# Kernel tuning notes

Hardware: AMD Instinct MI355X
Metric: run time of the kernel (lower is better)

The kernel has to match this reference:

```python
import jax, jax.numpy as jnp
import numpy as np

N = 50000
E = 800000
G = 64  # number of graphs in each batch
IN_DIM = 128
HID = 64
NEG_SLOPE = 0.2


def _glorot(key, shape):
    fan = shape[0] + shape[-1] if len(shape) == 2 else int(np.prod(shape[1:])) + shape[-1]
    lim = float(np.sqrt(6.0 / fan))
    return jax.random.uniform(key, shape, jnp.float32, -lim, lim)


def setup_inputs() -> dict:
    key = jax.random.key(0)
    ks = jax.random.split(key, 16)
    x1 = jax.random.normal(ks[0], (N, IN_DIM), jnp.float32)
    x2 = jax.random.normal(ks[1], (N, IN_DIM), jnp.float32)
    edge_index1 = jax.random.randint(ks[2], (2, E), 0, N, jnp.int64)
    edge_index2 = jax.random.randint(ks[3], (2, E), 0, N, jnp.int64)
    batch1 = jnp.sort(jax.random.randint(ks[4], (N,), 0, G, jnp.int64))
    batch2 = jnp.sort(jax.random.randint(ks[5], (N,), 0, G, jnp.int64))
    # conv1: GATConv(IN_DIM, HID, heads=4)
    W1 = _glorot(ks[6], (IN_DIM, 4 * HID))
    a_src1 = _glorot(ks[7], (1, 4, HID))
    a_dst1 = _glorot(ks[8], (1, 4, HID))
    b1 = jnp.zeros((4 * HID,), jnp.float32)
    # conv2: GATConv(4*HID, HID, heads=1)
    W2 = _glorot(ks[9], (4 * HID, HID))
    a_src2 = _glorot(ks[10], (1, 1, HID))
    a_dst2 = _glorot(ks[11], (1, 1, HID))
    b2 = jnp.zeros((HID,), jnp.float32)
    return {"x1": x1, "edge_index1": edge_index1, "batch1": batch1,
            "x2": x2, "edge_index2": edge_index2, "batch2": batch2,
            "W1": W1, "a_src1": a_src1, "a_dst1": a_dst1, "b1": b1,
            "W2": W2, "a_src2": a_src2, "a_dst2": a_dst2, "b2": b2}


def gat_conv(x, src, dst, W, a_src, a_dst, b, n_nodes, heads, out_dim):
    """PyG GATConv with add_self_loops=True, negative_slope=0.2, concat=True."""
    h = (x @ W).reshape(n_nodes, heads, out_dim)            # [N,H,D]
    alpha_s = jnp.sum(h * a_src, axis=-1)                   # [N,H]
    alpha_d = jnp.sum(h * a_dst, axis=-1)                   # [N,H]
    e = alpha_s[src] + alpha_d[dst]                         # [E',H]
    e = jax.nn.leaky_relu(e, NEG_SLOPE)
    # segment softmax over incoming edges of each destination node
    e_max = jax.ops.segment_max(e, dst, num_segments=n_nodes)
    ex = jnp.exp(e - e_max[dst])
    denom = jax.ops.segment_sum(ex, dst, num_segments=n_nodes)
    alpha = ex / (denom[dst] + 1e-16)                       # [E',H]
    msg = h[src] * alpha[:, :, None]                        # [E',H,D]
    out = jax.ops.segment_sum(msg, dst, num_segments=n_nodes)
    return out.reshape(n_nodes, heads * out_dim) + b


def embed(x, edge_index, batch, W1, a_src1, a_dst1, b1, W2, a_src2, a_dst2, b2):
    loops = jnp.arange(N, dtype=edge_index.dtype)
    src = jnp.concatenate([edge_index[0], loops])
    dst = jnp.concatenate([edge_index[1], loops])
    h = jax.nn.elu(gat_conv(x, src, dst, W1, a_src1, a_dst1, b1, N, 4, HID))
    h = jax.nn.elu(gat_conv(h, src, dst, W2, a_src2, a_dst2, b2, N, 1, HID))
    # global_mean_pool over graph ids
    sums = jax.ops.segment_sum(h, batch, num_segments=G)
    cnt = jax.ops.segment_sum(jnp.ones((N,), h.dtype), batch, num_segments=G)
    return sums / jnp.maximum(cnt, 1.0)[:, None]


def reference(x1, edge_index1, batch1, x2, edge_index2, batch2,
              W1, a_src1, a_dst1, b1, W2, a_src2, a_dst2, b2):
    emb1 = embed(x1, edge_index1, batch1, W1, a_src1, a_dst1, b1, W2, a_src2, a_dst2, b2)
    emb2 = embed(x2, edge_index2, batch2, W1, a_src1, a_dst1, b1, W2, a_src2, a_dst2, b2)
    return (emb1, emb2)
```

## Files before the change

kernel.cpp:

```cpp
#include <hip/hip_runtime.h>
#include <cstdint>
#include <cstddef>

#define NNODES 50000
#define NEDGES 800000
#define NGR    64
#define INDIM  128
#define HIDD   64

typedef __attribute__((ext_vector_type(8))) short bf16x8;
typedef __attribute__((ext_vector_type(4))) float f32x4;

__device__ __forceinline__ float lrelu(float x) { return x > 0.f ? x : 0.2f * x; }
__device__ __forceinline__ float eluf(float x)  { return x > 0.f ? x : expm1f(x); }
__device__ __forceinline__ float bf2f(unsigned short u) {
    return __uint_as_float((unsigned int)u << 16);
}
__device__ __forceinline__ unsigned short f2bf(float x) {
    unsigned int u = __float_as_uint(x);
    return (unsigned short)((u + 0x7fffu + ((u >> 16) & 1u)) >> 16);
}
__device__ __forceinline__ float lo16(unsigned int u) { return __uint_as_float(u << 16); }
__device__ __forceinline__ float hi16(unsigned int u) { return __uint_as_float(u & 0xffff0000u); }

__global__ void cvt_f2b(const float* __restrict__ in, unsigned short* __restrict__ out, int n4) {
    int i = blockIdx.x * 256 + threadIdx.x;
    if (i < n4) {
        float4 v = ((const float4*)in)[i];
        ushort4 o;
        o.x = f2bf(v.x); o.y = f2bf(v.y); o.z = f2bf(v.z); o.w = f2bf(v.w);
        ((ushort4*)out)[i] = o;
    }
}

__global__ void count_dst(const int* __restrict__ ei0, const int* __restrict__ ei1,
                          int* __restrict__ cnt, int E, int N) {
    const int* ei = blockIdx.y ? ei1 : ei0;
    int* c = cnt + blockIdx.y * N;
    int e = blockIdx.x * 256 + threadIdx.x;
    if (e < E) atomicAdd(&c[ei[E + e]], 1);
}

__global__ __launch_bounds__(256) void scan_part(const int* __restrict__ cnt,
                                                 int* __restrict__ psum, int n) {
    __shared__ int ws[4];
    const int* c = cnt + blockIdx.y * n;
    int* p = psum + blockIdx.y * 256;
    int lane = threadIdx.x & 63, w = threadIdx.x >> 6;
    int i = blockIdx.x * 256 + threadIdx.x;
    int v = (i < n) ? c[i] : 0;
    #pragma unroll
    for (int off = 32; off >= 1; off >>= 1) v += __shfl_xor(v, off, 64);
    if (lane == 0) ws[w] = v;
    __syncthreads();
    if (threadIdx.x == 0) p[blockIdx.x] = ws[0] + ws[1] + ws[2] + ws[3];
}

__global__ __launch_bounds__(256) void scan_tops(int* __restrict__ psum,
                                                 int* __restrict__ rp, int nb, int n) {
    __shared__ int wsum[4];
    int* p = psum + blockIdx.x * 256;
    int* r = rp + blockIdx.x * (n + 1);
    int tid = threadIdx.x, lane = tid & 63, w = tid >> 6;
    int v = (tid < nb) ? p[tid] : 0;
    int x = v;
    #pragma unroll
    for (int off = 1; off < 64; off <<= 1) {
        int t = __shfl_up(x, off, 64);
        if (lane >= off) x += t;
    }
    if (lane == 63) wsum[w] = x;
    __syncthreads();
    int add = 0;
    for (int k = 0; k < w; k++) add += wsum[k];
    int incl = x + add;
    if (tid < nb) p[tid] = incl - v;
    if (tid == nb - 1) r[n] = incl;
}

__global__ __launch_bounds__(256) void scan_fin(const int* __restrict__ cnt,
                                                const int* __restrict__ psum,
                                                int* __restrict__ rp, int n) {
    __shared__ int wsum[4];
    const int* c = cnt + blockIdx.y * n;
    const int* p = psum + blockIdx.y * 256;
    int* r = rp + blockIdx.y * (n + 1);
    int tid = threadIdx.x, lane = tid & 63, w = tid >> 6;
    int i = blockIdx.x * 256 + tid;
    int v = (i < n) ? c[i] : 0;
    int x = v;
    #pragma unroll
    for (int off = 1; off < 64; off <<= 1) {
        int t = __shfl_up(x, off, 64);
        if (lane >= off) x += t;
    }
    if (lane == 63) wsum[w] = x;
    __syncthreads();
    int add = p[blockIdx.x];
    for (int k = 0; k < w; k++) add += wsum[k];
    if (i < n) r[i] = x + add - v;
}

__global__ void fill_csr(const int* __restrict__ ei0, const int* __restrict__ ei1,
                         const int* __restrict__ rp, int* __restrict__ fc,
                         int* __restrict__ col, int E, int N) {
    int g = blockIdx.y;
    const int* ei = g ? ei1 : ei0;
    const int* r = rp + g * (N + 1);
    int* f = fc + g * N;
    int* cl = col + (size_t)g * E;
    int e = blockIdx.x * 256 + threadIdx.x;
    if (e < E) {
        int s = ei[e];
        int d = ei[E + e];
        int pos = atomicAdd(&f[d], 1);
        cl[r[d] + pos] = s;
    }
}

template<int BN, int WM, int WN, bool AF32>
__global__ __launch_bounds__(256) void gemm_mfma(const void* __restrict__ A0,
                                                 const void* __restrict__ A1,
                                                 size_t Ags,
                                                 const unsigned short* __restrict__ Bw,
                                                 unsigned short* __restrict__ C,
                                                 size_t Cgs,
                                                 int M, int K, int N,
                                                 const float* __restrict__ a_src,
                                                 const float* __restrict__ a_dst,
                                                 float* __restrict__ as_o,
                                                 float* __restrict__ ad_o,
                                                 int hstride, int ags) {
    constexpr int BM = 128, BK = 64;
    constexpr int MI = WM / 16, NI = WN / 16;
    constexpr int LDA = BK + 8;
    __shared__ unsigned short Asm[BM * LDA];
    __shared__ unsigned short Bsm[BN * LDA];
    int gph = blockIdx.z;
    const float* Af = (const float*)(gph ? A1 : A0);
    const unsigned short* Ab = (const unsigned short*)A0 + (size_t)gph * Ags;
    unsigned short* Cg = C + (size_t)gph * Cgs;
    float* aso = as_o + (size_t)gph * ags;
    float* ado = ad_o + (size_t)gph * ags;
    int tid = threadIdx.x;
    int lane = tid & 63, wave = tid >> 6;
    int l15 = lane & 15, quad = lane >> 4;
    int wm0, wn0;
    if (BN == 128) { wm0 = (wave >> 1) * 64; wn0 = (wave & 1) * 64; }
    else           { wm0 = wave * 32;        wn0 = 0; }
    int row0 = blockIdx.x * BM;
    int c0 = blockIdx.y * BN;

    f32x4 acc[MI][NI];
    #pragma unroll
    for (int mi = 0; mi < MI; mi++)
        #pragma unroll
        for (int ni = 0; ni < NI; ni++)
            acc[mi][ni] = (f32x4){0.f, 0.f, 0.f, 0.f};

    for (int k0 = 0; k0 < K; k0 += BK) {
        #pragma unroll
        for (int q = 0; q < BM / 32; q++) {
            int idx = q * 256 + tid;
            int r = idx >> 3, kc = idx & 7;
            int row = row0 + r;
            if (AF32) {
                float4 v0 = make_float4(0.f, 0.f, 0.f, 0.f), v1 = v0;
                if (row < M) {
                    v0 = *(const float4*)(Af + (size_t)row * K + k0 + kc * 8);
                    v1 = *(const float4*)(Af + (size_t)row * K + k0 + kc * 8 + 4);
                }
                unsigned short t[8] = {f2bf(v0.x), f2bf(v0.y), f2bf(v0.z), f2bf(v0.w),
                                       f2bf(v1.x), f2bf(v1.y), f2bf(v1.z), f2bf(v1.w)};
                *(uint4*)&Asm[r * LDA + kc * 8] = *(uint4*)t;
            } else {
                uint4 v = make_uint4(0u, 0u, 0u, 0u);
                if (row < M) v = *(const uint4*)(Ab + (size_t)row * K + k0 + kc * 8);
                *(uint4*)&Asm[r * LDA + kc * 8] = v;
            }
        }
        #pragma unroll
        for (int q = 0; q < BN / 32; q++) {
            int idx = q * 256 + tid;
            int n  = idx & (BN - 1);
            int kc = idx / BN;
            unsigned short tmp[8];
            #pragma unroll
            for (int j = 0; j < 8; j++)
                tmp[j] = Bw[(size_t)(k0 + kc * 8 + j) * N + c0 + n];
            *(uint4*)&Bsm[n * LDA + kc * 8] = *(uint4*)tmp;
        }
        __syncthreads();
        #pragma unroll
        for (int kb = 0; kb < 2; kb++) {
            bf16x8 af[MI], bfr[NI];
            #pragma unroll
            for (int mi = 0; mi < MI; mi++)
                af[mi] = *(bf16x8*)&Asm[(wm0 + mi * 16 + l15) * LDA + kb * 32 + quad * 8];
            #pragma unroll
            for (int ni = 0; ni < NI; ni++)
                bfr[ni] = *(bf16x8*)&Bsm[(wn0 + ni * 16 + l15) * LDA + kb * 32 + quad * 8];
            #pragma unroll
            for (int mi = 0; mi < MI; mi++)
                #pragma unroll
                for (int ni = 0; ni < NI; ni++)
                    acc[mi][ni] = __builtin_amdgcn_mfma_f32_16x16x32_bf16(
                        af[mi], bfr[ni], acc[mi][ni], 0, 0, 0);
        }
        __syncthreads();
    }
    #pragma unroll
    for (int mi = 0; mi < MI; mi++) {
        #pragma unroll
        for (int r = 0; r < 4; r++) {
            int row = row0 + wm0 + mi * 16 + quad * 4 + r;
            if (row < M) {
                #pragma unroll
                for (int ni = 0; ni < NI; ni++) {
                    int colg = c0 + wn0 + ni * 16 + l15;
                    Cg[(size_t)row * N + colg] = f2bf(acc[mi][ni][r]);
                }
            }
        }
    }
    int headc = (c0 + wn0) >> 6;
    float a_s[NI], a_d[NI];
    #pragma unroll
    for (int ni = 0; ni < NI; ni++) {
        a_s[ni] = a_src[headc * 64 + ni * 16 + l15];
        a_d[ni] = a_dst[headc * 64 + ni * 16 + l15];
    }
    #pragma unroll
    for (int mi = 0; mi < MI; mi++) {
        #pragma unroll
        for (int r = 0; r < 4; r++) {
            float ps = 0.f, pd = 0.f;
            #pragma unroll
            for (int ni = 0; ni < NI; ni++) {
                ps += acc[mi][ni][r] * a_s[ni];
                pd += acc[mi][ni][r] * a_d[ni];
            }
            #pragma unroll
            for (int off = 1; off < 16; off <<= 1) {
                ps += __shfl_xor(ps, off, 64);
                pd += __shfl_xor(pd, off, 64);
            }
            int row = row0 + wm0 + mi * 16 + quad * 4 + r;
            if (l15 == 0 && row < M) {
                aso[row * hstride + headc] = ps;
                ado[row * hstride + headc] = pd;
            }
        }
    }
}

__global__ __launch_bounds__(256) void agg_h4(const unsigned short* __restrict__ h,
                                              size_t hgs,
                                              const float* __restrict__ as_,
                                              const float* __restrict__ ad_, int ags,
                                              const int* __restrict__ rp,
                                              const int* __restrict__ col,
                                              const float* __restrict__ bias,
                                              unsigned short* __restrict__ out,
                                              size_t ogs, int n, int E) {
    int gph = blockIdx.y;
    const uint4* h4 = (const uint4*)(h + (size_t)gph * hgs);
    const float* as = as_ + (size_t)gph * ags;
    const float* adp = ad_ + (size_t)gph * ags;
    const int* r = rp + gph * (n + 1);
    const int* cl = col + (size_t)gph * E;
    unsigned short* og = out + (size_t)gph * ogs;

    int wave = threadIdx.x >> 6, lane = threadIdx.x & 63;
    int node = blockIdx.x * 4 + wave;
    if (node >= n) return;
    int p = lane >> 5;
    int c = lane & 31;
    int headc = c >> 3;
    int l15 = lane & 15, quad = lane >> 4;
    float adv_q = adp[node * 4 + quad];
    float w0 = __expf(lrelu(as[node * 4 + headc] + adp[node * 4 + headc]));
    float m0 = (p == 0) ? w0 : 0.f;
    uint4 hu = h4[(size_t)node * 32 + c];
    float den = m0;
    float a0 = lo16(hu.x) * m0, a1 = hi16(hu.x) * m0;
    float a2 = lo16(hu.y) * m0, a3 = hi16(hu.y) * m0;
    float a4 = lo16(hu.z) * m0, a5 = hi16(hu.z) * m0;
    float a6 = lo16(hu.w) * m0, a7 = hi16(hu.w) * m0;
    int beg = __builtin_amdgcn_readfirstlane(r[node]);
    int end = __builtin_amdgcn_readfirstlane(r[node + 1]);
    int hbase = headc << 4;
    for (int j = beg; j < end; j += 16) {
        int m = end - j; if (m > 16) m = 16;
        int colv = cl[j + (l15 < m ? l15 : m - 1)];
        float wl = __expf(lrelu(as[colv * 4 + quad] + adv_q));
        for (int base = 0; base < m; base += 2) {
            int e = base + p;
            int ec = e < m ? e : m - 1;
            float we = __shfl(wl, hbase | ec);
            if (e >= m) we = 0.f;
            int s = __shfl(colv, ec);
            uint4 u = h4[(size_t)s * 32 + c];
            den += we;
            a0 += lo16(u.x) * we; a1 += hi16(u.x) * we;
            a2 += lo16(u.y) * we; a3 += hi16(u.y) * we;
            a4 += lo16(u.z) * we; a5 += hi16(u.z) * we;
            a6 += lo16(u.w) * we; a7 += hi16(u.w) * we;
        }
    }
    den += __shfl_xor(den, 32);
    a0 += __shfl_xor(a0, 32); a1 += __shfl_xor(a1, 32);
    a2 += __shfl_xor(a2, 32); a3 += __shfl_xor(a3, 32);
    a4 += __shfl_xor(a4, 32); a5 += __shfl_xor(a5, 32);
    a6 += __shfl_xor(a6, 32); a7 += __shfl_xor(a7, 32);
    if (p == 0) {
        float rden = 1.f / (den + 1e-16f);
        float4 b0 = ((const float4*)bias)[c * 2];
        float4 b1 = ((const float4*)bias)[c * 2 + 1];
        unsigned short t[8];
        t[0] = f2bf(eluf(a0 * rden + b0.x)); t[1] = f2bf(eluf(a1 * rden + b0.y));
        t[2] = f2bf(eluf(a2 * rden + b0.z)); t[3] = f2bf(eluf(a3 * rden + b0.w));
        t[4] = f2bf(eluf(a4 * rden + b1.x)); t[5] = f2bf(eluf(a5 * rden + b1.y));
        t[6] = f2bf(eluf(a6 * rden + b1.z)); t[7] = f2bf(eluf(a7 * rden + b1.w));
        ((uint4*)(og + (size_t)node * 256))[c] = *(uint4*)t;
    }
}

__global__ __launch_bounds__(256) void agg_h1(const unsigned short* __restrict__ h,
                                              size_t hgs,
                                              const float* __restrict__ as_,
                                              const float* __restrict__ ad_,
                                              const int* __restrict__ rp,
                                              const int* __restrict__ col,
                                              const float* __restrict__ bias,
                                              float* __restrict__ out,
                                              size_t ogs, int n, int E) {
    int gph = blockIdx.y;
    const uint4* h4 = (const uint4*)(h + (size_t)gph * hgs);
    const float* as = as_ + (size_t)gph * n;
    const float* adp = ad_ + (size_t)gph * n;
    const int* r = rp + gph * (n + 1);
    const int* cl = col + (size_t)gph * E;
    float* og = out + (size_t)gph * ogs;

    int wave = threadIdx.x >> 6, lane = threadIdx.x & 63;
    int node = blockIdx.x * 4 + wave;
    if (node >= n) return;
    int p = lane >> 3;
    int c = lane & 7;
    float adv = adp[node];
    float w0 = __expf(lrelu(as[node] + adv));
    float m0 = (p == 0) ? w0 : 0.f;
    uint4 hu = h4[(size_t)node * 8 + c];
    float den = m0;
    float a0 = lo16(hu.x) * m0, a1 = hi16(hu.x) * m0;
    float a2 = lo16(hu.y) * m0, a3 = hi16(hu.y) * m0;
    float a4 = lo16(hu.z) * m0, a5 = hi16(hu.z) * m0;
    float a6 = lo16(hu.w) * m0, a7 = hi16(hu.w) * m0;
    int beg = __builtin_amdgcn_readfirstlane(r[node]);
    int end = __builtin_amdgcn_readfirstlane(r[node + 1]);
    for (int j = beg; j < end; j += 64) {
        int m = end - j; if (m > 64) m = 64;
        int colv = cl[j + (lane < m ? lane : m - 1)];
        float wl = __expf(lrelu(as[colv] + adv));
        for (int base = 0; base < m; base += 8) {
            int e = base + p;
            int ec = e < m ? e : m - 1;
            float we = __shfl(wl, ec);
            if (e >= m) we = 0.f;
            int s = __shfl(colv, ec);
            uint4 u = h4[(size_t)s * 8 + c];
            den += we;
            a0 += lo16(u.x) * we; a1 += hi16(u.x) * we;
            a2 += lo16(u.y) * we; a3 += hi16(u.y) * we;
            a4 += lo16(u.z) * we; a5 += hi16(u.z) * we;
            a6 += lo16(u.w) * we; a7 += hi16(u.w) * we;
        }
    }
    #pragma unroll
    for (int off = 8; off < 64; off <<= 1) {
        den += __shfl_xor(den, off);
        a0 += __shfl_xor(a0, off); a1 += __shfl_xor(a1, off);
        a2 += __shfl_xor(a2, off); a3 += __shfl_xor(a3, off);
        a4 += __shfl_xor(a4, off); a5 += __shfl_xor(a5, off);
        a6 += __shfl_xor(a6, off); a7 += __shfl_xor(a7, off);
    }
    if (p == 0) {
        float rden = 1.f / (den + 1e-16f);
        float4 b0 = ((const float4*)bias)[c * 2];
        float4 b1 = ((const float4*)bias)[c * 2 + 1];
        float4 o0, o1;
        o0.x = eluf(a0 * rden + b0.x); o0.y = eluf(a1 * rden + b0.y);
        o0.z = eluf(a2 * rden + b0.z); o0.w = eluf(a3 * rden + b0.w);
        o1.x = eluf(a4 * rden + b1.x); o1.y = eluf(a5 * rden + b1.y);
        o1.z = eluf(a6 * rden + b1.z); o1.w = eluf(a7 * rden + b1.w);
        float* orow = og + (size_t)node * 64 + c * 8;
        *(float4*)orow = o0;
        *(float4*)(orow + 4) = o1;
    }
}

__device__ __forceinline__ int lbound(const int* __restrict__ a, int n, int key) {
    int lo = 0, hi = n;
    while (lo < hi) {
        int mid = (lo + hi) >> 1;
        if (a[mid] < key) lo = mid + 1; else hi = mid;
    }
    return lo;
}

__global__ __launch_bounds__(256) void pool_mean(const float* __restrict__ g2,
                                                 size_t ggs,
                                                 const int* __restrict__ b0,
                                                 const int* __restrict__ b1,
                                                 float* __restrict__ out, int n) {
    __shared__ float red[4][64];
    __shared__ int bnds[2];
    int gph = blockIdx.y;
    const int* batch = gph ? b1 : b0;
    const float* gg = g2 + (size_t)gph * ggs;
    float* og = out + (size_t)gph * NGR * HIDD;
    int g = blockIdx.x;
    if (threadIdx.x < 2) bnds[threadIdx.x] = lbound(batch, n, g + (int)threadIdx.x);
    __syncthreads();
    int s = bnds[0], e = bnds[1];
    int lane = threadIdx.x & 63, wave = threadIdx.x >> 6;
    float acc = 0.f;
    for (int i = s + wave; i < e; i += 4)
        acc += gg[(size_t)i * 64 + lane];
    red[wave][lane] = acc;
    __syncthreads();
    if (wave == 0) {
        float sum = red[0][lane] + red[1][lane] + red[2][lane] + red[3][lane];
        og[g * 64 + lane] = sum / fmaxf((float)(e - s), 1.0f);
    }
}

extern "C" void kernel_launch(void* const* d_in, const int* in_sizes, int n_in,
                              void* d_out, int out_size, void* d_ws, size_t ws_size,
                              hipStream_t stream) {
    const int N = NNODES, E = NEDGES;

    const float* x1 = (const float*)d_in[0];
    const float* x2 = (const float*)d_in[3];
    const int* ei1v = (const int*)d_in[1];
    const int* ei2v = (const int*)d_in[4];
    const int* ba1  = (const int*)d_in[2];
    const int* ba2  = (const int*)d_in[5];
    const float* W1     = (const float*)d_in[6];
    const float* a_src1 = (const float*)d_in[7];
    const float* a_dst1 = (const float*)d_in[8];
    const float* b1     = (const float*)d_in[9];
    const float* W2     = (const float*)d_in[10];
    const float* a_src2 = (const float*)d_in[11];
    const float* a_dst2 = (const float*)d_in[12];
    const float* b2     = (const float*)d_in[13];

    char* ws = (char*)d_ws;
    size_t off = 0;
    auto carve = [&](size_t bytes) -> char* {
        char* p = ws + off;
        off = (off + bytes + 255) & ~(size_t)255;
        return p;
    };
    char* R1 = carve((size_t)2 * N * 256 * 2);
    char* R2 = carve((size_t)2 * N * 256 * 2);
    char* R3 = carve((size_t)2 * N * 64 * 2);
    int*   col  = (int*)carve((size_t)2 * E * 4);
    int*   rp   = (int*)carve((size_t)2 * (N + 1) * 4);
    int*   cntN = (int*)carve((size_t)2 * N * 4);
    int*   psum = (int*)carve(2 * 256 * 4);
    float* as1  = (float*)carve((size_t)2 * N * 4 * 4);
    float* ad1  = (float*)carve((size_t)2 * N * 4 * 4);
    float* as2  = (float*)carve((size_t)2 * N * 4);
    float* ad2  = (float*)carve((size_t)2 * N * 4);
    unsigned short* W1b = (unsigned short*)carve(INDIM * 256 * 2);
    unsigned short* W2b = (unsigned short*)carve(256 * HIDD * 2);

    unsigned short* h1 = (unsigned short*)R1;
    unsigned short* g1 = (unsigned short*)R2;
    unsigned short* h2 = (unsigned short*)R3;
    float* g2 = (float*)R1;

    float* outF = (float*)d_out;

    const int nodeBlocks = (N + 3) / 4;
    const int nb = (N + 255) / 256;
    const int eb = (E + 255) / 256;

    cvt_f2b<<<(INDIM * 256 / 4 + 255) / 256, 256, 0, stream>>>(W1, W1b, INDIM * 256 / 4);
    cvt_f2b<<<(256 * HIDD / 4 + 255) / 256, 256, 0, stream>>>(W2, W2b, 256 * HIDD / 4);

    hipMemsetAsync(cntN, 0, (size_t)2 * N * 4, stream);
    count_dst<<<dim3(eb, 2), 256, 0, stream>>>(ei1v, ei2v, cntN, E, N);
    scan_part<<<dim3(nb, 2), 256, 0, stream>>>(cntN, psum, N);
    scan_tops<<<2, 256, 0, stream>>>(psum, rp, nb, N);
    scan_fin<<<dim3(nb, 2), 256, 0, stream>>>(cntN, psum, rp, N);
    hipMemsetAsync(cntN, 0, (size_t)2 * N * 4, stream);
    fill_csr<<<dim3(eb, 2), 256, 0, stream>>>(ei1v, ei2v, rp, cntN, col, E, N);

    gemm_mfma<128, 64, 64, true><<<dim3(391, 2, 2), 256, 0, stream>>>(
        x1, x2, 0, W1b, h1, (size_t)N * 256, N, INDIM, 256,
        a_src1, a_dst1, as1, ad1, 4, N * 4);
    agg_h4<<<dim3(nodeBlocks, 2), 256, 0, stream>>>(h1, (size_t)N * 256, as1, ad1, N * 4,
                                                    rp, col, b1, g1, (size_t)N * 256, N, E);

    gemm_mfma<64, 32, 64, false><<<dim3(391, 1, 2), 256, 0, stream>>>(
        g1, nullptr, (size_t)N * 256, W2b, h2, (size_t)N * 64, N, 256, HIDD,
        a_src2, a_dst2, as2, ad2, 1, N);
    agg_h1<<<dim3(nodeBlocks, 2), 256, 0, stream>>>(h2, (size_t)N * 64, as2, ad2,
                                                    rp, col, b2, g2, (size_t)N * 64, N, E);

    pool_mean<<<dim3(NGR, 2), 256, 0, stream>>>(g2, (size_t)N * 64, ba1, ba2, outF, N);
}
```

Baseline: 575.3 us.

## Software-pipeline GAT aggregation gathers and widen per-lane feature slices in layer 0

In the layer-0 aggregation kernel, each lane now handles 16 features (two uint4 loads) and the wave processes four edges at a time instead of two. In both aggregation kernels the next edge's feature row and the next chunk's column indices and source attention scores are prefetched before the current ones are accumulated. The aim is to hide gather latency and issue more memory requests in flight. The cost is more live registers (16 accumulators plus the prefetched vectors), which can lower occupancy.

```diff
diff --git a/kernel.cpp b/kernel.cpp
--- a/kernel.cpp
+++ b/kernel.cpp
@@ -274,55 +274,108 @@
     int wave = threadIdx.x >> 6, lane = threadIdx.x & 63;
     int node = blockIdx.x * 4 + wave;
     if (node >= n) return;
-    int p = lane >> 5;
-    int c = lane & 31;
-    int headc = c >> 3;
-    int l15 = lane & 15, quad = lane >> 4;
-    float adv_q = adp[node * 4 + quad];
+    int p = lane >> 4;
+    int c = lane & 15;
+    int headc = c >> 2;
+    float adv_q = adp[node * 4 + p];
     float w0 = __expf(lrelu(as[node * 4 + headc] + adp[node * 4 + headc]));
     float m0 = (p == 0) ? w0 : 0.f;
-    uint4 hu = h4[(size_t)node * 32 + c];
+    uint4 hu0 = h4[(size_t)node * 32 + 2 * c];
+    uint4 hu1 = h4[(size_t)node * 32 + 2 * c + 1];
     float den = m0;
-    float a0 = lo16(hu.x) * m0, a1 = hi16(hu.x) * m0;
-    float a2 = lo16(hu.y) * m0, a3 = hi16(hu.y) * m0;
-    float a4 = lo16(hu.z) * m0, a5 = hi16(hu.z) * m0;
-    float a6 = lo16(hu.w) * m0, a7 = hi16(hu.w) * m0;
+    float a0  = lo16(hu0.x) * m0, a1  = hi16(hu0.x) * m0;
+    float a2  = lo16(hu0.y) * m0, a3  = hi16(hu0.y) * m0;
+    float a4  = lo16(hu0.z) * m0, a5  = hi16(hu0.z) * m0;
+    float a6  = lo16(hu0.w) * m0, a7  = hi16(hu0.w) * m0;
+    float a8  = lo16(hu1.x) * m0, a9  = hi16(hu1.x) * m0;
+    float a10 = lo16(hu1.y) * m0, a11 = hi16(hu1.y) * m0;
+    float a12 = lo16(hu1.z) * m0, a13 = hi16(hu1.z) * m0;
+    float a14 = lo16(hu1.w) * m0, a15 = hi16(hu1.w) * m0;
     int beg = __builtin_amdgcn_readfirstlane(r[node]);
     int end = __builtin_amdgcn_readfirstlane(r[node + 1]);
     int hbase = headc << 4;
-    for (int j = beg; j < end; j += 16) {
-        int m = end - j; if (m > 16) m = 16;
-        int colv = cl[j + (l15 < m ? l15 : m - 1)];
-        float wl = __expf(lrelu(as[colv * 4 + quad] + adv_q));
-        for (int base = 0; base < m; base += 2) {
-            int e = base + p;
-            int ec = e < m ? e : m - 1;
-            float we = __shfl(wl, hbase | ec);
-            if (e >= m) we = 0.f;
-            int s = __shfl(colv, ec);
-            uint4 u = h4[(size_t)s * 32 + c];
+    int j = beg;
+    int m = end - j; if (m > 16) m = 16;
+    int colv = 0; float asv = 0.f;
+    if (j < end) {
+        colv = cl[j + (c < m ? c : m - 1)];
+        asv = as[colv * 4 + p];
+    }
+    while (j < end) {
+        int jn = j + 16;
+        int mn = end - jn; if (mn > 16) mn = 16;
+        int colv_n = 0; float asv_n = 0.f;
+        if (mn > 0) {
+            colv_n = cl[jn + (c < mn ? c : mn - 1)];
+            asv_n = as[colv_n * 4 + p];
+        }
+        float wl = __expf(lrelu(asv + adv_q));
+        int e0 = p;
+        int ec = e0 < m ? e0 : m - 1;
+        float we = __shfl(wl, hbase | ec);
+        if (e0 >= m) we = 0.f;
+        int s = __shfl(colv, ec);
+        uint4 u0 = h4[(size_t)s * 32 + 2 * c];
+        uint4 u1 = h4[(size_t)s * 32 + 2 * c + 1];
+        for (int base = 4; base < m; base += 4) {
+            int e2 = base + p;
+            int ec2 = e2 < m ? e2 : m - 1;
+            float we2 = __shfl(wl, hbase | ec2);
+            if (e2 >= m) we2 = 0.f;
+            int s2 = __shfl(colv, ec2);
+            uint4 v0 = h4[(size_t)s2 * 32 + 2 * c];
+            uint4 v1 = h4[(size_t)s2 * 32 + 2 * c + 1];
             den += we;
-            a0 += lo16(u.x) * we; a1 += hi16(u.x) * we;
-            a2 += lo16(u.y) * we; a3 += hi16(u.y) * we;
-            a4 += lo16(u.z) * we; a5 += hi16(u.z) * we;
-            a6 += lo16(u.w) * we; a7 += hi16(u.w) * we;
-        }
-    }
-    den += __shfl_xor(den, 32);
-    a0 += __shfl_xor(a0, 32); a1 += __shfl_xor(a1, 32);
-    a2 += __shfl_xor(a2, 32); a3 += __shfl_xor(a3, 32);
-    a4 += __shfl_xor(a4, 32); a5 += __shfl_xor(a5, 32);
-    a6 += __shfl_xor(a6, 32); a7 += __shfl_xor(a7, 32);
+            a0  += lo16(u0.x) * we; a1  += hi16(u0.x) * we;
+            a2  += lo16(u0.y) * we; a3  += hi16(u0.y) * we;
+            a4  += lo16(u0.z) * we; a5  += hi16(u0.z) * we;
+            a6  += lo16(u0.w) * we; a7  += hi16(u0.w) * we;
+            a8  += lo16(u1.x) * we; a9  += hi16(u1.x) * we;
+            a10 += lo16(u1.y) * we; a11 += hi16(u1.y) * we;
+            a12 += lo16(u1.z) * we; a13 += hi16(u1.z) * we;
+            a14 += lo16(u1.w) * we; a15 += hi16(u1.w) * we;
+            we = we2; u0 = v0; u1 = v1;
+        }
+        den += we;
+        a0  += lo16(u0.x) * we; a1  += hi16(u0.x) * we;
+        a2  += lo16(u0.y) * we; a3  += hi16(u0.y) * we;
+        a4  += lo16(u0.z) * we; a5  += hi16(u0.z) * we;
+        a6  += lo16(u0.w) * we; a7  += hi16(u0.w) * we;
+        a8  += lo16(u1.x) * we; a9  += hi16(u1.x) * we;
+        a10 += lo16(u1.y) * we; a11 += hi16(u1.y) * we;
+        a12 += lo16(u1.z) * we; a13 += hi16(u1.z) * we;
+        a14 += lo16(u1.w) * we; a15 += hi16(u1.w) * we;
+        j = jn; m = mn; colv = colv_n; asv = asv_n;
+    }
+    #pragma unroll
+    for (int off = 16; off < 64; off <<= 1) {
+        den += __shfl_xor(den, off);
+        a0  += __shfl_xor(a0,  off); a1  += __shfl_xor(a1,  off);
+        a2  += __shfl_xor(a2,  off); a3  += __shfl_xor(a3,  off);
+        a4  += __shfl_xor(a4,  off); a5  += __shfl_xor(a5,  off);
+        a6  += __shfl_xor(a6,  off); a7  += __shfl_xor(a7,  off);
+        a8  += __shfl_xor(a8,  off); a9  += __shfl_xor(a9,  off);
+        a10 += __shfl_xor(a10, off); a11 += __shfl_xor(a11, off);
+        a12 += __shfl_xor(a12, off); a13 += __shfl_xor(a13, off);
+        a14 += __shfl_xor(a14, off); a15 += __shfl_xor(a15, off);
+    }
     if (p == 0) {
         float rden = 1.f / (den + 1e-16f);
-        float4 b0 = ((const float4*)bias)[c * 2];
-        float4 b1 = ((const float4*)bias)[c * 2 + 1];
-        unsigned short t[8];
-        t[0] = f2bf(eluf(a0 * rden + b0.x)); t[1] = f2bf(eluf(a1 * rden + b0.y));
-        t[2] = f2bf(eluf(a2 * rden + b0.z)); t[3] = f2bf(eluf(a3 * rden + b0.w));
-        t[4] = f2bf(eluf(a4 * rden + b1.x)); t[5] = f2bf(eluf(a5 * rden + b1.y));
-        t[6] = f2bf(eluf(a6 * rden + b1.z)); t[7] = f2bf(eluf(a7 * rden + b1.w));
-        ((uint4*)(og + (size_t)node * 256))[c] = *(uint4*)t;
+        const float4* b4 = (const float4*)bias;
+        float4 b0 = b4[c * 4], b1 = b4[c * 4 + 1];
+        float4 b2 = b4[c * 4 + 2], b3 = b4[c * 4 + 3];
+        unsigned short t[16];
+        t[0]  = f2bf(eluf(a0  * rden + b0.x)); t[1]  = f2bf(eluf(a1  * rden + b0.y));
+        t[2]  = f2bf(eluf(a2  * rden + b0.z)); t[3]  = f2bf(eluf(a3  * rden + b0.w));
+        t[4]  = f2bf(eluf(a4  * rden + b1.x)); t[5]  = f2bf(eluf(a5  * rden + b1.y));
+        t[6]  = f2bf(eluf(a6  * rden + b1.z)); t[7]  = f2bf(eluf(a7  * rden + b1.w));
+        t[8]  = f2bf(eluf(a8  * rden + b2.x)); t[9]  = f2bf(eluf(a9  * rden + b2.y));
+        t[10] = f2bf(eluf(a10 * rden + b2.z)); t[11] = f2bf(eluf(a11 * rden + b2.w));
+        t[12] = f2bf(eluf(a12 * rden + b3.x)); t[13] = f2bf(eluf(a13 * rden + b3.y));
+        t[14] = f2bf(eluf(a14 * rden + b3.z)); t[15] = f2bf(eluf(a15 * rden + b3.w));
+        uint4* orow = (uint4*)(og + (size_t)node * 256);
+        orow[2 * c]     = *(uint4*)&t[0];
+        orow[2 * c + 1] = *(uint4*)&t[8];
     }
 }
 
@@ -359,23 +412,48 @@
     float a6 = lo16(hu.w) * m0, a7 = hi16(hu.w) * m0;
     int beg = __builtin_amdgcn_readfirstlane(r[node]);
     int end = __builtin_amdgcn_readfirstlane(r[node + 1]);
-    for (int j = beg; j < end; j += 64) {
-        int m = end - j; if (m > 64) m = 64;
-        int colv = cl[j + (lane < m ? lane : m - 1)];
-        float wl = __expf(lrelu(as[colv] + adv));
-        for (int base = 0; base < m; base += 8) {
-            int e = base + p;
-            int ec = e < m ? e : m - 1;
-            float we = __shfl(wl, ec);
-            if (e >= m) we = 0.f;
-            int s = __shfl(colv, ec);
-            uint4 u = h4[(size_t)s * 8 + c];
+    int j = beg;
+    int m = end - j; if (m > 64) m = 64;
+    int colv = 0; float asv = 0.f;
+    if (j < end) {
+        colv = cl[j + (lane < m ? lane : m - 1)];
+        asv = as[colv];
+    }
+    while (j < end) {
+        int jn = j + 64;
+        int mn = end - jn; if (mn > 64) mn = 64;
+        int colv_n = 0; float asv_n = 0.f;
+        if (mn > 0) {
+            colv_n = cl[jn + (lane < mn ? lane : mn - 1)];
+            asv_n = as[colv_n];
+        }
+        float wl = __expf(lrelu(asv + adv));
+        int e0 = p;
+        int ec = e0 < m ? e0 : m - 1;
+        float we = __shfl(wl, ec);
+        if (e0 >= m) we = 0.f;
+        int s = __shfl(colv, ec);
+        uint4 u = h4[(size_t)s * 8 + c];
+        for (int base = 8; base < m; base += 8) {
+            int e2 = base + p;
+            int ec2 = e2 < m ? e2 : m - 1;
+            float we2 = __shfl(wl, ec2);
+            if (e2 >= m) we2 = 0.f;
+            int s2 = __shfl(colv, ec2);
+            uint4 u2 = h4[(size_t)s2 * 8 + c];
             den += we;
             a0 += lo16(u.x) * we; a1 += hi16(u.x) * we;
             a2 += lo16(u.y) * we; a3 += hi16(u.y) * we;
             a4 += lo16(u.z) * we; a5 += hi16(u.z) * we;
             a6 += lo16(u.w) * we; a7 += hi16(u.w) * we;
-        }
+            we = we2; u = u2;
+        }
+        den += we;
+        a0 += lo16(u.x) * we; a1 += hi16(u.x) * we;
+        a2 += lo16(u.y) * we; a3 += hi16(u.y) * we;
+        a4 += lo16(u.z) * we; a5 += hi16(u.z) * we;
+        a6 += lo16(u.w) * we; a7 += hi16(u.w) * we;
+        j = jn; m = mn; colv = colv_n; asv = asv_n;
     }
     #pragma unroll
     for (int off = 8; off < 64; off <<= 1) {
```

New measurement: 571.7 us. No clear change (-0.6%).

## Aggregate raw inputs before projection in first GAT layer and switch to fp16

Applied to the files above, without the earlier changes.

Layer one is reordered so neighbor aggregation runs over the 128-wide fp16 input features instead of the 256-wide projected features. Per-head attention logits come from x times a precomputed W1·a vector, and the per-head aggregated inputs are then multiplied by W1 in a GEMM that also applies bias and ELU. This cuts the bytes gathered per edge in the largest gather, but it writes four per-head aggregated copies and adds extra kernels. The change also moves all 16-bit storage and MFMA from bf16 to fp16, which adds overflow and precision risk.

```diff
diff --git a/kernel.cpp b/kernel.cpp
--- a/kernel.cpp
+++ b/kernel.cpp
@@ -8,28 +8,90 @@
 #define INDIM  128
 #define HIDD   64
 
-typedef __attribute__((ext_vector_type(8))) short bf16x8;
+typedef __attribute__((ext_vector_type(8))) _Float16 f16x8;
+typedef __attribute__((ext_vector_type(2))) _Float16 half2v;
 typedef __attribute__((ext_vector_type(4))) float f32x4;
 
 __device__ __forceinline__ float lrelu(float x) { return x > 0.f ? x : 0.2f * x; }
 __device__ __forceinline__ float eluf(float x)  { return x > 0.f ? x : expm1f(x); }
-__device__ __forceinline__ float bf2f(unsigned short u) {
-    return __uint_as_float((unsigned int)u << 16);
-}
-__device__ __forceinline__ unsigned short f2bf(float x) {
-    unsigned int u = __float_as_uint(x);
-    return (unsigned short)((u + 0x7fffu + ((u >> 16) & 1u)) >> 16);
-}
-__device__ __forceinline__ float lo16(unsigned int u) { return __uint_as_float(u << 16); }
-__device__ __forceinline__ float hi16(unsigned int u) { return __uint_as_float(u & 0xffff0000u); }
-
-__global__ void cvt_f2b(const float* __restrict__ in, unsigned short* __restrict__ out, int n4) {
+__device__ __forceinline__ unsigned short f2h(float x) {
+    _Float16 h = (_Float16)x;
+    return __builtin_bit_cast(unsigned short, h);
+}
+__device__ __forceinline__ float h2f(unsigned short u) {
+    return (float)__builtin_bit_cast(_Float16, u);
+}
+__device__ __forceinline__ float h2lo(unsigned int u) {
+    half2v h = __builtin_bit_cast(half2v, u);
+    return (float)h.x;
+}
+__device__ __forceinline__ float h2hi(unsigned int u) {
+    half2v h = __builtin_bit_cast(half2v, u);
+    return (float)h.y;
+}
+
+__global__ void cvt_f2h(const float* __restrict__ in, unsigned short* __restrict__ out, int n4) {
     int i = blockIdx.x * 256 + threadIdx.x;
     if (i < n4) {
         float4 v = ((const float4*)in)[i];
         ushort4 o;
-        o.x = f2bf(v.x); o.y = f2bf(v.y); o.z = f2bf(v.z); o.w = f2bf(v.w);
+        o.x = f2h(v.x); o.y = f2h(v.y); o.z = f2h(v.z); o.w = f2h(v.w);
         ((ushort4*)out)[i] = o;
+    }
+}
+
+__global__ __launch_bounds__(256) void proj_ws(const float* __restrict__ W1f,
+                                               const float* __restrict__ a_src,
+                                               const float* __restrict__ a_dst,
+                                               float* __restrict__ proj) {
+    int o = blockIdx.x * 256 + threadIdx.x;
+    if (o >= 1024) return;
+    int sd = o >> 9, h = (o >> 7) & 3, k = o & 127;
+    const float* av = sd ? a_dst : a_src;
+    float s = 0.f;
+    #pragma unroll 8
+    for (int d = 0; d < 64; d++)
+        s += W1f[k * 256 + h * 64 + d] * av[h * 64 + d];
+    proj[o] = s;
+}
+
+__global__ __launch_bounds__(256) void cvt_xa(const float* __restrict__ x0,
+                                              const float* __restrict__ x1,
+                                              const float* __restrict__ proj,
+                                              unsigned short* __restrict__ x16,
+                                              float* __restrict__ as1,
+                                              float* __restrict__ ad1, int n) {
+    int gph = blockIdx.y;
+    const float* xf = (gph ? x1 : x0);
+    unsigned short* xo = x16 + (size_t)gph * n * 128;
+    float* aso = as1 + (size_t)gph * n * 4;
+    float* ado = ad1 + (size_t)gph * n * 4;
+    int wave = threadIdx.x >> 6, lane = threadIdx.x & 63;
+    int node = blockIdx.x * 4 + wave;
+    if (node >= n) return;
+    float2 v = *(const float2*)(xf + (size_t)node * 128 + lane * 2);
+    ushort2 t; t.x = f2h(v.x); t.y = f2h(v.y);
+    *(unsigned int*)(xo + (size_t)node * 128 + lane * 2) =
+        __builtin_bit_cast(unsigned int, t);
+    float ps[4], pd[4];
+    #pragma unroll
+    for (int h = 0; h < 4; h++) {
+        float2 ws = *(const float2*)(proj + h * 128 + lane * 2);
+        float2 wd = *(const float2*)(proj + 512 + h * 128 + lane * 2);
+        ps[h] = v.x * ws.x + v.y * ws.y;
+        pd[h] = v.x * wd.x + v.y * wd.y;
+    }
+    #pragma unroll
+    for (int off = 1; off < 64; off <<= 1) {
+        #pragma unroll
+        for (int h = 0; h < 4; h++) {
+            ps[h] += __shfl_xor(ps[h], off, 64);
+            pd[h] += __shfl_xor(pd[h], off, 64);
+        }
+    }
+    if (lane == 0) {
+        *(float4*)(aso + node * 4) = make_float4(ps[0], ps[1], ps[2], ps[3]);
+        *(float4*)(ado + node * 4) = make_float4(pd[0], pd[1], pd[2], pd[3]);
     }
 }
 
@@ -118,9 +180,165 @@
     }
 }
 
-template<int BN, int WM, int WN, bool AF32>
-__global__ __launch_bounds__(256) void gemm_mfma(const void* __restrict__ A0,
-                                                 const void* __restrict__ A1,
+__global__ __launch_bounds__(256) void agg_x4(const unsigned short* __restrict__ x16,
+                                              const float* __restrict__ as_,
+                                              const float* __restrict__ ad_,
+                                              const int* __restrict__ rp,
+                                              const int* __restrict__ col,
+                                              unsigned short* __restrict__ z,
+                                              int n, int E, int gph) {
+    const unsigned short* xg = x16 + (size_t)gph * n * 128;
+    const float* as = as_ + (size_t)gph * n * 4;
+    const float* adp = ad_ + (size_t)gph * n * 4;
+    const int* r = rp + gph * (n + 1);
+    const int* cl = col + (size_t)gph * E;
+
+    int wave = threadIdx.x >> 6, lane = threadIdx.x & 63;
+    int node = blockIdx.x * 4 + wave;
+    if (node >= n) return;
+    int p = lane >> 5;
+    int c = lane & 31;
+    int l15 = lane & 15, quad = lane >> 4;
+    float adv_q = adp[node * 4 + quad];
+
+    float w0[4];
+    #pragma unroll
+    for (int h = 0; h < 4; h++)
+        w0[h] = __expf(lrelu(as[node * 4 + h] + adp[node * 4 + h]));
+    uint2 hu = *(const uint2*)(xg + (size_t)node * 128 + c * 4);
+    float x0 = h2lo(hu.x), x1v = h2hi(hu.x), x2v = h2lo(hu.y), x3v = h2hi(hu.y);
+    float den[4], acc[4][4];
+    #pragma unroll
+    for (int h = 0; h < 4; h++) {
+        float m0 = (p == 0) ? w0[h] : 0.f;
+        den[h] = m0;
+        acc[h][0] = x0 * m0; acc[h][1] = x1v * m0;
+        acc[h][2] = x2v * m0; acc[h][3] = x3v * m0;
+    }
+    int beg = __builtin_amdgcn_readfirstlane(r[node]);
+    int end = __builtin_amdgcn_readfirstlane(r[node + 1]);
+    for (int j = beg; j < end; j += 16) {
+        int m = end - j; if (m > 16) m = 16;
+        int colv = cl[j + (l15 < m ? l15 : m - 1)];
+        float wl = __expf(lrelu(as[colv * 4 + quad] + adv_q));
+        for (int base = 0; base < m; base += 2) {
+            int e = base + p;
+            int ec = e < m ? e : m - 1;
+            int s = __shfl(colv, ec);
+            uint2 u = *(const uint2*)(xg + (size_t)s * 128 + c * 4);
+            float f0 = h2lo(u.x), f1 = h2hi(u.x), f2v = h2lo(u.y), f3 = h2hi(u.y);
+            #pragma unroll
+            for (int h = 0; h < 4; h++) {
+                float we = __shfl(wl, (h << 4) | ec);
+                if (e >= m) we = 0.f;
+                den[h] += we;
+                acc[h][0] = fmaf(f0, we, acc[h][0]);
+                acc[h][1] = fmaf(f1, we, acc[h][1]);
+                acc[h][2] = fmaf(f2v, we, acc[h][2]);
+                acc[h][3] = fmaf(f3, we, acc[h][3]);
+            }
+        }
+    }
+    #pragma unroll
+    for (int h = 0; h < 4; h++) {
+        den[h] += __shfl_xor(den[h], 32);
+        #pragma unroll
+        for (int k = 0; k < 4; k++) acc[h][k] += __shfl_xor(acc[h][k], 32);
+    }
+    if (p == 0) {
+        #pragma unroll
+        for (int h = 0; h < 4; h++) {
+            float rden = 1.f / (den[h] + 1e-16f);
+            ushort4 t;
+            t.x = f2h(acc[h][0] * rden); t.y = f2h(acc[h][1] * rden);
+            t.z = f2h(acc[h][2] * rden); t.w = f2h(acc[h][3] * rden);
+            *(uint2*)(z + ((size_t)h * n + node) * 128 + c * 4) = *(uint2*)&t;
+        }
+    }
+}
+
+__global__ __launch_bounds__(256) void gemm_z(const unsigned short* __restrict__ z,
+                                              const unsigned short* __restrict__ W1h,
+                                              const float* __restrict__ bias,
+                                              unsigned short* __restrict__ g1,
+                                              int M, int gph) {
+    constexpr int BM = 128, BK = 64, LDA = BK + 8;
+    __shared__ unsigned short Asm[BM * LDA];
+    __shared__ unsigned short Bsm[64 * LDA];
+    int h = blockIdx.z;
+    const unsigned short* Az = z + (size_t)h * M * 128;
+    unsigned short* Cg = g1 + (size_t)gph * M * 256;
+    int c0 = h * 64;
+    int tid = threadIdx.x, lane = tid & 63, wave = tid >> 6;
+    int l15 = lane & 15, quad = lane >> 4;
+    int wm0 = wave * 32;
+    int row0 = blockIdx.x * BM;
+
+    f32x4 acc[2][4];
+    #pragma unroll
+    for (int mi = 0; mi < 2; mi++)
+        #pragma unroll
+        for (int ni = 0; ni < 4; ni++)
+            acc[mi][ni] = (f32x4){0.f, 0.f, 0.f, 0.f};
+
+    for (int k0 = 0; k0 < 128; k0 += BK) {
+        #pragma unroll
+        for (int q = 0; q < 4; q++) {
+            int idx = q * 256 + tid;
+            int r = idx >> 3, kc = idx & 7;
+            int row = row0 + r;
+            uint4 v = make_uint4(0u, 0u, 0u, 0u);
+            if (row < M) v = *(const uint4*)(Az + (size_t)row * 128 + k0 + kc * 8);
+            *(uint4*)&Asm[r * LDA + kc * 8] = v;
+        }
+        #pragma unroll
+        for (int q = 0; q < 2; q++) {
+            int idx = q * 256 + tid;
+            int n = idx & 63;
+            int kc = idx >> 6;
+            unsigned short tmp[8];
+            #pragma unroll
+            for (int j = 0; j < 8; j++)
+                tmp[j] = W1h[(size_t)(k0 + kc * 8 + j) * 256 + c0 + n];
+            *(uint4*)&Bsm[n * LDA + kc * 8] = *(uint4*)tmp;
+        }
+        __syncthreads();
+        #pragma unroll
+        for (int kb = 0; kb < 2; kb++) {
+            f16x8 af[2], bfr[4];
+            #pragma unroll
+            for (int mi = 0; mi < 2; mi++)
+                af[mi] = *(f16x8*)&Asm[(wm0 + mi * 16 + l15) * LDA + kb * 32 + quad * 8];
+            #pragma unroll
+            for (int ni = 0; ni < 4; ni++)
+                bfr[ni] = *(f16x8*)&Bsm[(ni * 16 + l15) * LDA + kb * 32 + quad * 8];
+            #pragma unroll
+            for (int mi = 0; mi < 2; mi++)
+                #pragma unroll
+                for (int ni = 0; ni < 4; ni++)
+                    acc[mi][ni] = __builtin_amdgcn_mfma_f32_16x16x32_f16(
+                        af[mi], bfr[ni], acc[mi][ni], 0, 0, 0);
+        }
+        __syncthreads();
+    }
+    #pragma unroll
+    for (int mi = 0; mi < 2; mi++) {
+        #pragma unroll
+        for (int r = 0; r < 4; r++) {
+            int row = row0 + wm0 + mi * 16 + quad * 4 + r;
+            if (row < M) {
+                #pragma unroll
+                for (int ni = 0; ni < 4; ni++) {
+                    int colg = c0 + ni * 16 + l15;
+                    Cg[(size_t)row * 256 + colg] = f2h(eluf(acc[mi][ni][r] + bias[colg]));
+                }
+            }
+        }
+    }
+}
+
+template<int BN, int WM, int WN>
+__global__ __launch_bounds__(256) void gemm_mfma(const unsigned short* __restrict__ A0,
                                                  size_t Ags,
                                                  const unsigned short* __restrict__ Bw,
                                                  unsigned short* __restrict__ C,
@@ -137,17 +355,14 @@
     __shared__ unsigned short Asm[BM * LDA];
     __shared__ unsigned short Bsm[BN * LDA];
     int gph = blockIdx.z;
-    const float* Af = (const float*)(gph ? A1 : A0);
-    const unsigned short* Ab = (const unsigned short*)A0 + (size_t)gph * Ags;
+    const unsigned short* Ab = A0 + (size_t)gph * Ags;
     unsigned short* Cg = C + (size_t)gph * Cgs;
     float* aso = as_o + (size_t)gph * ags;
     float* ado = ad_o + (size_t)gph * ags;
     int tid = threadIdx.x;
     int lane = tid & 63, wave = tid >> 6;
     int l15 = lane & 15, quad = lane >> 4;
-    int wm0, wn0;
-    if (BN == 128) { wm0 = (wave >> 1) * 64; wn0 = (wave & 1) * 64; }
-    else           { wm0 = wave * 32;        wn0 = 0; }
+    int wm0 = wave * 32, wn0 = 0;
     int row0 = blockIdx.x * BM;
     int c0 = blockIdx.y * BN;
 
@@ -164,20 +379,9 @@
             int idx = q * 256 + tid;
             int r = idx >> 3, kc = idx & 7;
             int row = row0 + r;
-            if (AF32) {
-                float4 v0 = make_float4(0.f, 0.f, 0.f, 0.f), v1 = v0;
-                if (row < M) {
-                    v0 = *(const float4*)(Af + (size_t)row * K + k0 + kc * 8);
-                    v1 = *(const float4*)(Af + (size_t)row * K + k0 + kc * 8 + 4);
-                }
-                unsigned short t[8] = {f2bf(v0.x), f2bf(v0.y), f2bf(v0.z), f2bf(v0.w),
-                                       f2bf(v1.x), f2bf(v1.y), f2bf(v1.z), f2bf(v1.w)};
-                *(uint4*)&Asm[r * LDA + kc * 8] = *(uint4*)t;
-            } else {
-                uint4 v = make_uint4(0u, 0u, 0u, 0u);
-                if (row < M) v = *(const uint4*)(Ab + (size_t)row * K + k0 + kc * 8);
-                *(uint4*)&Asm[r * LDA + kc * 8] = v;
-            }
+            uint4 v = make_uint4(0u, 0u, 0u, 0u);
+            if (row < M) v = *(const uint4*)(Ab + (size_t)row * K + k0 + kc * 8);
+            *(uint4*)&Asm[r * LDA + kc * 8] = v;
         }
         #pragma unroll
         for (int q = 0; q < BN / 32; q++) {
@@ -193,18 +397,18 @@
         __syncthreads();
         #pragma unroll
         for (int kb = 0; kb < 2; kb++) {
-            bf16x8 af[MI], bfr[NI];
+            f16x8 af[MI], bfr[NI];
             #pragma unroll
             for (int mi = 0; mi < MI; mi++)
-                af[mi] = *(bf16x8*)&Asm[(wm0 + mi * 16 + l15) * LDA + kb * 32 + quad * 8];
+                af[mi] = *(f16x8*)&Asm[(wm0 + mi * 16 + l15) * LDA + kb * 32 + quad * 8];
             #pragma unroll
             for (int ni = 0; ni < NI; ni++)
-                bfr[ni] = *(bf16x8*)&Bsm[(wn0 + ni * 16 + l15) * LDA + kb * 32 + quad * 8];
+                bfr[ni] = *(f16x8*)&Bsm[(wn0 + ni * 16 + l15) * LDA + kb * 32 + quad * 8];
             #pragma unroll
             for (int mi = 0; mi < MI; mi++)
                 #pragma unroll
                 for (int ni = 0; ni < NI; ni++)
-                    acc[mi][ni] = __builtin_amdgcn_mfma_f32_16x16x32_bf16(
+                    acc[mi][ni] = __builtin_amdgcn_mfma_f32_16x16x32_f16(
                         af[mi], bfr[ni], acc[mi][ni], 0, 0, 0);
         }
         __syncthreads();
@@ -218,7 +422,7 @@
                 #pragma unroll
                 for (int ni = 0; ni < NI; ni++) {
                     int colg = c0 + wn0 + ni * 16 + l15;
-                    Cg[(size_t)row * N + colg] = f2bf(acc[mi][ni][r]);
+                    Cg[(size_t)row * N + colg] = f2h(acc[mi][ni][r]);
                 }
             }
         }
@@ -251,78 +455,6 @@
                 ado[row * hstride + headc] = pd;
             }
         }
-    }
-}
-
-__global__ __launch_bounds__(256) void agg_h4(const unsigned short* __restrict__ h,
-                                              size_t hgs,
-                                              const float* __restrict__ as_,
-                                              const float* __restrict__ ad_, int ags,
-                                              const int* __restrict__ rp,
-                                              const int* __restrict__ col,
-                                              const float* __restrict__ bias,
-                                              unsigned short* __restrict__ out,
-                                              size_t ogs, int n, int E) {
-    int gph = blockIdx.y;
-    const uint4* h4 = (const uint4*)(h + (size_t)gph * hgs);
-    const float* as = as_ + (size_t)gph * ags;
-    const float* adp = ad_ + (size_t)gph * ags;
-    const int* r = rp + gph * (n + 1);
-    const int* cl = col + (size_t)gph * E;
-    unsigned short* og = out + (size_t)gph * ogs;
-
-    int wave = threadIdx.x >> 6, lane = threadIdx.x & 63;
-    int node = blockIdx.x * 4 + wave;
-    if (node >= n) return;
-    int p = lane >> 5;
-    int c = lane & 31;
-    int headc = c >> 3;
-    int l15 = lane & 15, quad = lane >> 4;
-    float adv_q = adp[node * 4 + quad];
-    float w0 = __expf(lrelu(as[node * 4 + headc] + adp[node * 4 + headc]));
-    float m0 = (p == 0) ? w0 : 0.f;
-    uint4 hu = h4[(size_t)node * 32 + c];
-    float den = m0;
-    float a0 = lo16(hu.x) * m0, a1 = hi16(hu.x) * m0;
-    float a2 = lo16(hu.y) * m0, a3 = hi16(hu.y) * m0;
-    float a4 = lo16(hu.z) * m0, a5 = hi16(hu.z) * m0;
-    float a6 = lo16(hu.w) * m0, a7 = hi16(hu.w) * m0;
-    int beg = __builtin_amdgcn_readfirstlane(r[node]);
-    int end = __builtin_amdgcn_readfirstlane(r[node + 1]);
-    int hbase = headc << 4;
-    for (int j = beg; j < end; j += 16) {
-        int m = end - j; if (m > 16) m = 16;
-        int colv = cl[j + (l15 < m ? l15 : m - 1)];
-        float wl = __expf(lrelu(as[colv * 4 + quad] + adv_q));
-        for (int base = 0; base < m; base += 2) {
-            int e = base + p;
-            int ec = e < m ? e : m - 1;
-            float we = __shfl(wl, hbase | ec);
-            if (e >= m) we = 0.f;
-            int s = __shfl(colv, ec);
-            uint4 u = h4[(size_t)s * 32 + c];
-            den += we;
-            a0 += lo16(u.x) * we; a1 += hi16(u.x) * we;
-            a2 += lo16(u.y) * we; a3 += hi16(u.y) * we;
-            a4 += lo16(u.z) * we; a5 += hi16(u.z) * we;
-            a6 += lo16(u.w) * we; a7 += hi16(u.w) * we;
-        }
-    }
-    den += __shfl_xor(den, 32);
-    a0 += __shfl_xor(a0, 32); a1 += __shfl_xor(a1, 32);
-    a2 += __shfl_xor(a2, 32); a3 += __shfl_xor(a3, 32);
-    a4 += __shfl_xor(a4, 32); a5 += __shfl_xor(a5, 32);
-    a6 += __shfl_xor(a6, 32); a7 += __shfl_xor(a7, 32);
-    if (p == 0) {
-        float rden = 1.f / (den + 1e-16f);
-        float4 b0 = ((const float4*)bias)[c * 2];
-        float4 b1 = ((const float4*)bias)[c * 2 + 1];
-        unsigned short t[8];
-        t[0] = f2bf(eluf(a0 * rden + b0.x)); t[1] = f2bf(eluf(a1 * rden + b0.y));
-        t[2] = f2bf(eluf(a2 * rden + b0.z)); t[3] = f2bf(eluf(a3 * rden + b0.w));
-        t[4] = f2bf(eluf(a4 * rden + b1.x)); t[5] = f2bf(eluf(a5 * rden + b1.y));
-        t[6] = f2bf(eluf(a6 * rden + b1.z)); t[7] = f2bf(eluf(a7 * rden + b1.w));
-        ((uint4*)(og + (size_t)node * 256))[c] = *(uint4*)t;
     }
 }
 
@@ -353,10 +485,10 @@
     float m0 = (p == 0) ? w0 : 0.f;
     uint4 hu = h4[(size_t)node * 8 + c];
     float den = m0;
-    float a0 = lo16(hu.x) * m0, a1 = hi16(hu.x) * m0;
-    float a2 = lo16(hu.y) * m0, a3 = hi16(hu.y) * m0;
-    float a4 = lo16(hu.z) * m0, a5 = hi16(hu.z) * m0;
-    float a6 = lo16(hu.w) * m0, a7 = hi16(hu.w) * m0;
+    float a0 = h2lo(hu.x) * m0, a1 = h2hi(hu.x) * m0;
+    float a2 = h2lo(hu.y) * m0, a3 = h2hi(hu.y) * m0;
+    float a4 = h2lo(hu.z) * m0, a5 = h2hi(hu.z) * m0;
+    float a6 = h2lo(hu.w) * m0, a7 = h2hi(hu.w) * m0;
     int beg = __builtin_amdgcn_readfirstlane(r[node]);
     int end = __builtin_amdgcn_readfirstlane(r[node + 1]);
     for (int j = beg; j < end; j += 64) {
@@ -371,10 +503,10 @@
             int s = __shfl(colv, ec);
             uint4 u = h4[(size_t)s * 8 + c];
             den += we;
-            a0 += lo16(u.x) * we; a1 += hi16(u.x) * we;
-            a2 += lo16(u.y) * we; a3 += hi16(u.y) * we;
-            a4 += lo16(u.z) * we; a5 += hi16(u.z) * we;
-            a6 += lo16(u.w) * we; a7 += hi16(u.w) * we;
+            a0 = fmaf(h2lo(u.x), we, a0); a1 = fmaf(h2hi(u.x), we, a1);
+            a2 = fmaf(h2lo(u.y), we, a2); a3 = fmaf(h2hi(u.y), we, a3);
+            a4 = fmaf(h2lo(u.z), we, a4); a5 = fmaf(h2hi(u.z), we, a5);
+            a6 = fmaf(h2lo(u.w), we, a6); a7 = fmaf(h2hi(u.w), we, a7);
         }
     }
     #pragma unroll
@@ -463,9 +595,9 @@
         off = (off + bytes + 255) & ~(size_t)255;
         return p;
     };
-    char* R1 = carve((size_t)2 * N * 256 * 2);
-    char* R2 = carve((size_t)2 * N * 256 * 2);
-    char* R3 = carve((size_t)2 * N * 64 * 2);
+    unsigned short* x16 = (unsigned short*)carve((size_t)2 * N * 128 * 2);
+    char* Rz = carve((size_t)4 * N * 128 * 2);
+    unsigned short* g1 = (unsigned short*)carve((size_t)2 * N * 256 * 2);
     int*   col  = (int*)carve((size_t)2 * E * 4);
     int*   rp   = (int*)carve((size_t)2 * (N + 1) * 4);
     int*   cntN = (int*)carve((size_t)2 * N * 4);
@@ -474,13 +606,13 @@
     float* ad1  = (float*)carve((size_t)2 * N * 4 * 4);
     float* as2  = (float*)carve((size_t)2 * N * 4);
     float* ad2  = (float*)carve((size_t)2 * N * 4);
-    unsigned short* W1b = (unsigned short*)carve(INDIM * 256 * 2);
-    unsigned short* W2b = (unsigned short*)carve(256 * HIDD * 2);
-
-    unsigned short* h1 = (unsigned short*)R1;
-    unsigned short* g1 = (unsigned short*)R2;
-    unsigned short* h2 = (unsigned short*)R3;
-    float* g2 = (float*)R1;
+    float* proj = (float*)carve(2 * 4 * 128 * 4);
+    unsigned short* W1h = (unsigned short*)carve(INDIM * 256 * 2);
+    unsigned short* W2h = (unsigned short*)carve(256 * HIDD * 2);
+
+    unsigned short* zbuf = (unsigned short*)Rz;
+    float* g2 = (float*)Rz;
+    unsigned short* h2 = x16;
 
     float* outF = (float*)d_out;
 
@@ -488,8 +620,10 @@
     const int nb = (N + 255) / 256;
     const int eb = (E + 255) / 256;
 
-    cvt_f2b<<<(INDIM * 256 / 4 + 255) / 256, 256, 0, stream>>>(W1, W1b, INDIM * 256 / 4);
-    cvt_f2b<<<(256 * HIDD / 4 + 255) / 256, 256, 0, stream>>>(W2, W2b, 256 * HIDD / 4);
+    cvt_f2h<<<(INDIM * 256 / 4 + 255) / 256, 256, 0, stream>>>(W1, W1h, INDIM * 256 / 4);
+    cvt_f2h<<<(256 * HIDD / 4 + 255) / 256, 256, 0, stream>>>(W2, W2h, 256 * HIDD / 4);
+    proj_ws<<<4, 256, 0, stream>>>(W1, a_src1, a_dst1, proj);
+    cvt_xa<<<dim3(nodeBlocks, 2), 256, 0, stream>>>(x1, x2, proj, x16, as1, ad1, N);
 
     hipMemsetAsync(cntN, 0, (size_t)2 * N * 4, stream);
     count_dst<<<dim3(eb, 2), 256, 0, stream>>>(ei1v, ei2v, cntN, E, N);
@@ -499,14 +633,13 @@
     hipMemsetAsync(cntN, 0, (size_t)2 * N * 4, stream);
     fill_csr<<<dim3(eb, 2), 256, 0, stream>>>(ei1v, ei2v, rp, cntN, col, E, N);
 
-    gemm_mfma<128, 64, 64, true><<<dim3(391, 2, 2), 256, 0, stream>>>(
-        x1, x2, 0, W1b, h1, (size_t)N * 256, N, INDIM, 256,
-        a_src1, a_dst1, as1, ad1, 4, N * 4);
-    agg_h4<<<dim3(nodeBlocks, 2), 256, 0, stream>>>(h1, (size_t)N * 256, as1, ad1, N * 4,
-                                                    rp, col, b1, g1, (size_t)N * 256, N, E);
-
-    gemm_mfma<64, 32, 64, false><<<dim3(391, 1, 2), 256, 0, stream>>>(
-        g1, nullptr, (size_t)N * 256, W2b, h2, (size_t)N * 64, N, 256, HIDD,
+    agg_x4<<<nodeBlocks, 256, 0, stream>>>(x16, as1, ad1, rp, col, zbuf, N, E, 0);
+    gemm_z<<<dim3(391, 1, 4), 256, 0, stream>>>(zbuf, W1h, b1, g1, N, 0);
+    agg_x4<<<nodeBlocks, 256, 0, stream>>>(x16, as1, ad1, rp, col, zbuf, N, E, 1);
+    gemm_z<<<dim3(391, 1, 4), 256, 0, stream>>>(zbuf, W1h, b1, g1, N, 1);
+
+    gemm_mfma<64, 32, 64><<<dim3(391, 1, 2), 256, 0, stream>>>(
+        g1, (size_t)N * 256, W2h, h2, (size_t)N * 64, N, 256, HIDD,
         a_src2, a_dst2, as2, ad2, 1, N);
     agg_h1<<<dim3(nodeBlocks, 2), 256, 0, stream>>>(h2, (size_t)N * 64, as2, ad2,
                                                     rp, col, b2, g2, (size_t)N * 64, N, E);
```

New measurement: 606.8 us. 5.5% more time.
